# Kernel tuning notes

Measured on AMD Instinct MI355X. Metric: run time of the kernel, lower is better.

## Reference

```python
import jax, jax.numpy as jnp
import numpy as np

D_MODEL = 256
N_LAYERS = 2
EXPAND = 2
D_INNER = EXPAND * D_MODEL  # 512
D_STATE = 16
D_CONV = 4
DT_RANK = max(1, D_MODEL // 16)  # 16


def _selective_scan(x, dt, B, C, A, D):
    # x, dt: [b, l, d]   B, C: [b, l, n]   A: [d, n]   D: [d]
    dA = jnp.exp(jnp.einsum('bld,dn->bldn', dt, A))          # discretized state matrix
    dBx = jnp.einsum('bld,bln,bld->bldn', dt, B, x)           # dt * B * u

    def step(h, inp):
        dA_t, dBx_t, C_t = inp                                 # [b,d,n],[b,d,n],[b,n]
        h = dA_t * h + dBx_t
        y = jnp.einsum('bdn,bn->bd', h, C_t)
        return h, y

    h0 = jnp.zeros((x.shape[0], A.shape[0], A.shape[1]), x.dtype)
    _, ys = jax.lax.scan(step, h0, (jnp.moveaxis(dA, 1, 0),
                                    jnp.moveaxis(dBx, 1, 0),
                                    jnp.moveaxis(C, 1, 0)))
    return jnp.moveaxis(ys, 0, 1) + x * D                      # [b, l, d]


def _mamba_block(z, in_w, conv_w, conv_b, xp_w, dt_w, dt_b, A_log, Dp, out_w):
    b, l, _ = z.shape
    xz = z @ in_w.T                                            # [b, l, 2*d_inner]
    x, gate = jnp.split(xz, 2, axis=-1)
    # causal depthwise conv1d over time
    xt = jnp.transpose(x, (0, 2, 1))                            # [b, d_inner, l]
    xt = jax.lax.conv_general_dilated(
        xt, conv_w[:, None, :], window_strides=(1,),
        padding=[(D_CONV - 1, 0)], feature_group_count=D_INNER)
    x = jax.nn.silu(jnp.transpose(xt, (0, 2, 1)) + conv_b)      # [b, l, d_inner]
    x_dbl = x @ xp_w.T                                          # [b, l, dt_rank + 2*d_state]
    dt, Bm, Cm = jnp.split(x_dbl, [DT_RANK, DT_RANK + D_STATE], axis=-1)
    dt = jax.nn.softplus(dt @ dt_w.T + dt_b)                    # [b, l, d_inner]
    A = -jnp.exp(A_log)                                         # [d_inner, d_state]
    y = _selective_scan(x, dt, Bm, Cm, A, Dp)
    y = y * jax.nn.silu(gate)
    return y @ out_w.T                                          # [b, l, d_model]


def setup_inputs() -> dict:
    key = jax.random.key(0)
    ks = jax.random.split(key, 9)
    B, L = 2, 4096
    z = jax.random.normal(ks[0], (B, L, D_MODEL), jnp.float32)
    s = 0.02
    in_proj_w = jax.random.normal(ks[1], (N_LAYERS, 2 * D_INNER, D_MODEL), jnp.float32) * s
    conv_w = jax.random.normal(ks[2], (N_LAYERS, D_INNER, D_CONV), jnp.float32) * 0.2
    conv_b = jnp.zeros((N_LAYERS, D_INNER), jnp.float32)
    x_proj_w = jax.random.normal(ks[3], (N_LAYERS, DT_RANK + 2 * D_STATE, D_INNER), jnp.float32) * s
    dt_proj_w = jax.random.normal(ks[4], (N_LAYERS, D_INNER, DT_RANK), jnp.float32) * 0.1
    dt_proj_b = jax.random.uniform(ks[5], (N_LAYERS, D_INNER), jnp.float32, -4.0, -2.0)
    A_log = jnp.log(jnp.broadcast_to(jnp.arange(1, D_STATE + 1, dtype=jnp.float32),
                                     (N_LAYERS, D_INNER, D_STATE)))
    D_param = jnp.ones((N_LAYERS, D_INNER), jnp.float32)
    out_proj_w = jax.random.normal(ks[6], (N_LAYERS, D_MODEL, D_INNER), jnp.float32) * s
    return {"z": z, "in_proj_w": in_proj_w, "conv_w": conv_w, "conv_b": conv_b,
            "x_proj_w": x_proj_w, "dt_proj_w": dt_proj_w, "dt_proj_b": dt_proj_b,
            "A_log": A_log, "D_param": D_param, "out_proj_w": out_proj_w}


def reference(z, in_proj_w, conv_w, conv_b, x_proj_w, dt_proj_w, dt_proj_b,
              A_log, D_param, out_proj_w):
    for i in range(N_LAYERS):
        z = _mamba_block(z, in_proj_w[i], conv_w[i], conv_b[i], x_proj_w[i],
                         dt_proj_w[i], dt_proj_b[i], A_log[i], D_param[i], out_proj_w[i])
    return z
```

## Files before the change

### kernel.cpp

```cpp
#include <hip/hip_runtime.h>
#include <hip/hip_bf16.h>
#include <cstdint>
#include <cstddef>

#define DM   256
#define DI   512
#define DS   16
#define LSEQ 4096
#define BATCH 2
#define BLROWS (BATCH * LSEQ)
#define NCH  256
#define CLEN 16
#define NSC  16
#define XCP  520

typedef __bf16 bf16x8 __attribute__((ext_vector_type(8)));
typedef float  f32x4  __attribute__((ext_vector_type(4)));
typedef unsigned short u16;
typedef u16 u16x8 __attribute__((ext_vector_type(8)));

__device__ __forceinline__ u16 f2bfu(float f) {
    union { float f; unsigned u; } c; c.f = f;
    unsigned u = c.u;
    return (u16)((u + 0x7fffu + ((u >> 16) & 1u)) >> 16);
}
__device__ __forceinline__ float bfu2f(u16 u) {
    union { unsigned u; float f; } c; c.u = ((unsigned)u) << 16; return c.f;
}
__device__ __forceinline__ float siluf(float v) {
    return v * (1.0f / (1.0f + __expf(-v)));
}
__device__ __forceinline__ void gload_lds16(const void* g, void* l) {
    __builtin_amdgcn_global_load_lds(
        (const __attribute__((address_space(1))) unsigned int*)g,
        (__attribute__((address_space(3))) unsigned int*)l, 16, 0, 0);
}

#define POW_TREE(an, e1)                                                     \
    {   float e2 = (e1)*(e1), e4 = e2*e2, e8 = e4*e4;                        \
        an[0]=(e1); an[1]=e2; an[2]=e2*(e1); an[3]=e4; an[4]=e4*(e1);        \
        an[5]=e4*e2; an[6]=e4*an[2]; an[7]=e8; an[8]=e8*(e1); an[9]=e8*e2;   \
        an[10]=e8*an[2]; an[11]=e8*e4; an[12]=e8*an[4]; an[13]=e8*an[5];     \
        an[14]=e8*an[6]; an[15]=e8*e8; }

#define N_INW  (2*1024*256)
#define N_OUTW (2*256*512)
#define N_XPW  (2*64*512)
#define N_Z    (BLROWS*DM)
__global__ __launch_bounds__(256) void cast_all_k(
    const float* __restrict__ in_w, const float* __restrict__ out_w,
    const float* __restrict__ xp_w, const float* __restrict__ z,
    u16* __restrict__ inw_bf, u16* __restrict__ outw_bf,
    u16* __restrict__ xpw_bf, u16* __restrict__ z_bf) {
    int i = blockIdx.x * 256 + threadIdx.x;
    if (i < N_INW) {
        inw_bf[i] = f2bfu(in_w[i]);
    } else if (i < N_INW + N_OUTW) {
        int j = i - N_INW;
        outw_bf[j] = f2bfu(out_w[j]);
    } else if (i < N_INW + N_OUTW + N_XPW) {
        int j = i - (N_INW + N_OUTW);
        int k = j & 511, o = (j >> 9) & 63, l = j >> 15;
        xpw_bf[j] = f2bfu((o < 48) ? xp_w[(l * 48 + o) * 512 + k] : 0.0f);
    } else {
        int j = i - (N_INW + N_OUTW + N_XPW);
        z_bf[j] = f2bfu(z[j]);
    }
}

__global__ __launch_bounds__(256) void gemm_in_k(
    const __bf16* __restrict__ A, const __bf16* __restrict__ B,
    u16* __restrict__ Cb, int M, int N, int K) {
    __shared__ __bf16 As[128 * 32];
    __shared__ __bf16 Bs[128 * 32];
    int tid = threadIdx.x, wave = tid >> 6, lane = tid & 63;
    int bm = blockIdx.x * 128, bn = blockIdx.y * 128;
    int wm = (wave & 1) * 64, wn = (wave >> 1) * 64;
    int row = lane & 15, q = lane >> 4;
    int srow = lane >> 2, sseg = lane & 3;
    f32x4 acc[4][4] = {};
    for (int k0 = 0; k0 < K; k0 += 32) {
        #pragma unroll
        for (int i = 0; i < 2; ++i) {
            int r0 = wave * 32 + i * 16;
            gload_lds16(A + (size_t)(bm + r0 + srow) * K + k0 + sseg * 8, As + r0 * 32);
            gload_lds16(B + (size_t)(bn + r0 + srow) * K + k0 + sseg * 8, Bs + r0 * 32);
        }
        __syncthreads();
        bf16x8 af[4], bfr[4];
        #pragma unroll
        for (int mi = 0; mi < 4; ++mi)
            af[mi] = *(const bf16x8*)&As[(wm + mi*16 + row) * 32 + q * 8];
        #pragma unroll
        for (int ni = 0; ni < 4; ++ni)
            bfr[ni] = *(const bf16x8*)&Bs[(wn + ni*16 + row) * 32 + q * 8];
        #pragma unroll
        for (int mi = 0; mi < 4; ++mi)
            #pragma unroll
            for (int ni = 0; ni < 4; ++ni)
                acc[mi][ni] = __builtin_amdgcn_mfma_f32_16x16x32_bf16(
                    af[mi], bfr[ni], acc[mi][ni], 0, 0, 0);
        __syncthreads();
    }
    #pragma unroll
    for (int mi = 0; mi < 4; ++mi)
        #pragma unroll
        for (int r = 0; r < 4; ++r) {
            size_t gr = (size_t)(bm + wm + mi*16 + q*4 + r) * N;
            #pragma unroll
            for (int ni = 0; ni < 4; ++ni)
                Cb[gr + bn + wn + ni*16 + row] = f2bfu(acc[mi][ni][r]);
        }
}

__global__ __launch_bounds__(512, 6) void fused_a_k(
    const u16* __restrict__ xz, const float* __restrict__ cw,
    const float* __restrict__ cb, const __bf16* __restrict__ xpw,
    const float* __restrict__ dtw, const float* __restrict__ dtb,
    const float* __restrict__ Alog,
    u16* __restrict__ xcb, u16* __restrict__ dtob,
    float* __restrict__ BCg, u16* __restrict__ Pb, u16* __restrict__ Sb) {
    __shared__ u16 xc_s[CLEN * XCP];
    __shared__ float xd_h[2][CLEN * 68];
    int tid = threadIdx.x;
    int c = blockIdx.x, b = blockIdx.y;
    int flat = b * NCH + c;
    int bl0 = b * LSEQ + c * CLEN;
    int d = tid;

    {
        float w0 = cw[d*4], w1 = cw[d*4+1], w2 = cw[d*4+2], w3 = cw[d*4+3];
        float bias = cb[d];
        float xm3 = 0.f, xm2 = 0.f, xm1 = 0.f;
        int l0 = c * CLEN;
        if (l0 - 3 >= 0) xm3 = bfu2f(xz[(size_t)(bl0 - 3) * 1024 + d]);
        if (l0 - 2 >= 0) xm2 = bfu2f(xz[(size_t)(bl0 - 2) * 1024 + d]);
        if (l0 - 1 >= 0) xm1 = bfu2f(xz[(size_t)(bl0 - 1) * 1024 + d]);
        #pragma unroll 4
        for (int t = 0; t < CLEN; ++t) {
            float xcur = bfu2f(xz[(size_t)(bl0 + t) * 1024 + d]);
            float acc = fmaf(w0, xm3, fmaf(w1, xm2, fmaf(w2, xm1, fmaf(w3, xcur, bias))));
            float v = siluf(acc);
            u16 vb = f2bfu(v);
            xc_s[t * XCP + d] = vb;
            xcb[(size_t)(bl0 + t) * DI + d] = vb;
            xm3 = xm2; xm2 = xm1; xm1 = xcur;
        }
    }
    __syncthreads();

    {
        int wave = tid >> 6, lane = tid & 63;
        int row = lane & 15, q = lane >> 4;
        int nt = wave & 3, kh = wave >> 2;
        f32x4 acc = {0.f, 0.f, 0.f, 0.f};
        #pragma unroll
        for (int kb = 0; kb < 8; ++kb) {
            int kk = (kh*8 + kb) * 32;
            bf16x8 a = *(const bf16x8*)&xc_s[row * XCP + kk + q*8];
            bf16x8 bb = *(const bf16x8*)(xpw + (size_t)(nt*16 + row) * 512 + kk + q*8);
            acc = __builtin_amdgcn_mfma_f32_16x16x32_bf16(a, bb, acc, 0, 0, 0);
        }
        #pragma unroll
        for (int r = 0; r < 4; ++r)
            xd_h[kh][(q*4 + r) * 68 + nt*16 + row] = acc[r];
    }
    __syncthreads();
    for (int j = tid; j < CLEN * 68; j += 512) xd_h[0][j] += xd_h[1][j];
    __syncthreads();

    {
        int t = tid >> 5, cc = tid & 31;
        BCg[(size_t)flat * (CLEN*32) + tid] = xd_h[0][t*68 + 16 + cc];
    }

    {
        float dtwr[16];
        const f32x4* w4 = (const f32x4*)(dtw + (size_t)d * 16);
        #pragma unroll
        for (int g = 0; g < 4; ++g) { f32x4 v = w4[g];
            dtwr[g*4] = v[0]; dtwr[g*4+1] = v[1]; dtwr[g*4+2] = v[2]; dtwr[g*4+3] = v[3]; }
        float dtbv = dtb[d];
        float Ac0; bool fastp = true;
        {
            const f32x4* a4 = (const f32x4*)(Alog + (size_t)d * 16);
            f32x4 v0 = a4[0];
            Ac0 = -__expf(v0[0]);
            #pragma unroll
            for (int g = 0; g < 4; ++g) { f32x4 v = a4[g];
                #pragma unroll
                for (int j = 0; j < 4; ++j) { int n = g*4 + j; if (n) {
                    float acn = -__expf(v[j]);
                    fastp = fastp && (fabsf(acn - (float)(n+1)*Ac0) <= 1e-4f*fabsf(acn));
                } } }
        }
        float s[16];
        #pragma unroll
        for (int n = 0; n < 16; ++n) s[n] = 0.f;
        float Sdt = 0.f;
        if (fastp) {
            for (int t = 0; t < CLEN; ++t) {
                float acc = dtbv;
                #pragma unroll
                for (int r = 0; r < 16; ++r) acc = fmaf(xd_h[0][t*68 + r], dtwr[r], acc);
                float dtraw = (acc > 20.0f) ? acc : logf(1.0f + __expf(acc));
                u16 dtu = f2bfu(dtraw);
                dtob[(size_t)(bl0 + t) * DI + d] = dtu;
                float dtv = bfu2f(dtu);
                float xv = bfu2f(xc_s[t * XCP + d]);
                float dx = dtv * xv;
                Sdt += dtv;
                float e1 = __expf(dtv * Ac0);
                float an[16];
                POW_TREE(an, e1)
                #pragma unroll
                for (int n = 0; n < 16; ++n)
                    s[n] = fmaf(an[n], s[n], xd_h[0][t*68 + 16 + n] * dx);
            }
        } else {
            for (int t = 0; t < CLEN; ++t) {
                float acc = dtbv;
                #pragma unroll
                for (int r = 0; r < 16; ++r) acc = fmaf(xd_h[0][t*68 + r], dtwr[r], acc);
                float dtraw = (acc > 20.0f) ? acc : logf(1.0f + __expf(acc));
                u16 dtu = f2bfu(dtraw);
                dtob[(size_t)(bl0 + t) * DI + d] = dtu;
                float dtv = bfu2f(dtu);
                float xv = bfu2f(xc_s[t * XCP + d]);
                float dx = dtv * xv;
                Sdt += dtv;
                #pragma unroll
                for (int n = 0; n < 16; ++n) {
                    float an = __expf(dtv * -__expf(Alog[(size_t)d*16 + n]));
                    s[n] = fmaf(an, s[n], xd_h[0][t*68 + 16 + n] * dx);
                }
            }
        }
        float pw[16];
        if (fastp) {
            float E1 = __expf(Ac0 * Sdt);
            POW_TREE(pw, E1)
        } else {
            #pragma unroll
            for (int n = 0; n < 16; ++n)
                pw[n] = __expf(-__expf(Alog[(size_t)d*16 + n]) * Sdt);
        }
        size_t base = ((size_t)flat * DI + d) * 16;
        u16x8 pv0, pv1, sv0, sv1;
        #pragma unroll
        for (int n = 0; n < 8; ++n) {
            pv0[n] = f2bfu(pw[n]);  pv1[n] = f2bfu(pw[8+n]);
            sv0[n] = f2bfu(s[n]);   sv1[n] = f2bfu(s[8+n]);
        }
        *(u16x8*)(Pb + base)     = pv0;  *(u16x8*)(Pb + base + 8) = pv1;
        *(u16x8*)(Sb + base)     = sv0;  *(u16x8*)(Sb + base + 8) = sv1;
    }
}

__global__ __launch_bounds__(256) void scan1_k(
    const u16* __restrict__ Pb, const u16* __restrict__ Sb,
    float* __restrict__ Pagg, float* __restrict__ Sagg) {
    int gid = blockIdx.x * 256 + threadIdx.x;
    int scg = gid >> 13, elow = gid & 8191;
    int b = scg >> 4, sc = scg & 15;
    int cbase = b * NCH + sc * 16;
    float h = 0.f, p = 1.f;
    #pragma unroll
    for (int k = 0; k < 16; ++k) {
        size_t a = (size_t)(cbase + k) * 8192 + elow;
        float Pv = bfu2f(Pb[a]), Sv = bfu2f(Sb[a]);
        h = fmaf(Pv, h, Sv);
        p *= Pv;
    }
    Pagg[(size_t)scg * 8192 + elow] = p;
    Sagg[(size_t)scg * 8192 + elow] = h;
}

__global__ __launch_bounds__(256) void scan2_k(
    const u16* __restrict__ Pb, const u16* __restrict__ Sb,
    const float* __restrict__ Pagg, const float* __restrict__ Sagg,
    u16* __restrict__ Hg) {
    int gid = blockIdx.x * 256 + threadIdx.x;
    int scg = gid >> 13, elow = gid & 8191;
    int b = scg >> 4, sc = scg & 15;
    int cbase = b * NCH + sc * 16;
    float h = 0.f;
    for (int s2 = 0; s2 < sc; ++s2) {
        size_t ai = (size_t)(b*16 + s2) * 8192 + elow;
        h = fmaf(Pagg[ai], h, Sagg[ai]);
    }
    #pragma unroll
    for (int k = 0; k < 16; ++k) {
        size_t a = (size_t)(cbase + k) * 8192 + elow;
        Hg[a] = f2bfu(h);
        h = fmaf(bfu2f(Pb[a]), h, bfu2f(Sb[a]));
    }
}

__global__ __launch_bounds__(512, 6) void fused_c_k(
    const u16* __restrict__ xcb, const u16* __restrict__ dtob,
    const float* __restrict__ BCg, const u16* __restrict__ Hg,
    const float* __restrict__ Alog, const float* __restrict__ Dp,
    const u16* __restrict__ xz, const __bf16* __restrict__ outw,
    u16* __restrict__ Ob, float* __restrict__ Of) {
    __shared__ u16 y_s[CLEN * XCP];
    __shared__ float BCs[CLEN * 32];
    int tid = threadIdx.x;
    int c = blockIdx.x, b = blockIdx.y;
    int flat = b * NCH + c;
    int bl0 = b * LSEQ + c * CLEN;
    int d = tid;

    BCs[tid] = BCg[(size_t)flat * (CLEN*32) + tid];

    float Ac0; bool fastp = true;
    {
        const f32x4* a4 = (const f32x4*)(Alog + (size_t)d * 16);
        f32x4 v0 = a4[0];
        Ac0 = -__expf(v0[0]);
        #pragma unroll
        for (int g = 0; g < 4; ++g) { f32x4 v = a4[g];
            #pragma unroll
            for (int j = 0; j < 4; ++j) { int n = g*4 + j; if (n) {
                float acn = -__expf(v[j]);
                fastp = fastp && (fabsf(acn - (float)(n+1)*Ac0) <= 1e-4f*fabsf(acn));
            } } }
    }
    float h[16];
    {
        const u16* h8 = Hg + ((size_t)flat * DI + d) * 16;
        u16x8 hv0 = *(const u16x8*)h8;
        u16x8 hv1 = *(const u16x8*)(h8 + 8);
        #pragma unroll
        for (int n = 0; n < 8; ++n) { h[n] = bfu2f(hv0[n]); h[8+n] = bfu2f(hv1[n]); }
    }
    float Dv = Dp[d];
    __syncthreads();

    if (fastp) {
        for (int t = 0; t < CLEN; ++t) {
            float dtv = bfu2f(dtob[(size_t)(bl0 + t) * DI + d]);
            float xv  = bfu2f(xcb[(size_t)(bl0 + t) * DI + d]);
            float gv  = bfu2f(xz[(size_t)(bl0 + t) * 1024 + DI + d]);
            float dx = dtv * xv;
            float e1 = __expf(dtv * Ac0);
            float an[16];
            POW_TREE(an, e1)
            float y0 = 0.f, y1 = 0.f, y2 = 0.f, y3 = 0.f;
            #pragma unroll
            for (int n = 0; n < 4; ++n) {
                h[n]    = fmaf(an[n],    h[n],    BCs[t*32 + n]    * dx);
                h[4+n]  = fmaf(an[4+n],  h[4+n],  BCs[t*32 + 4+n]  * dx);
                h[8+n]  = fmaf(an[8+n],  h[8+n],  BCs[t*32 + 8+n]  * dx);
                h[12+n] = fmaf(an[12+n], h[12+n], BCs[t*32 + 12+n] * dx);
                y0 = fmaf(h[n],    BCs[t*32 + 16 + n],    y0);
                y1 = fmaf(h[4+n],  BCs[t*32 + 16 + 4+n],  y1);
                y2 = fmaf(h[8+n],  BCs[t*32 + 16 + 8+n],  y2);
                y3 = fmaf(h[12+n], BCs[t*32 + 16 + 12+n], y3);
            }
            float y = (y0 + y1) + (y2 + y3);
            float yv = fmaf(xv, Dv, y) * siluf(gv);
            y_s[t * XCP + d] = f2bfu(yv);
        }
    } else {
        for (int t = 0; t < CLEN; ++t) {
            float dtv = bfu2f(dtob[(size_t)(bl0 + t) * DI + d]);
            float xv  = bfu2f(xcb[(size_t)(bl0 + t) * DI + d]);
            float gv  = bfu2f(xz[(size_t)(bl0 + t) * 1024 + DI + d]);
            float dx = dtv * xv;
            float y = 0.f;
            #pragma unroll
            for (int n = 0; n < 16; ++n) {
                float an = __expf(dtv * -__expf(Alog[(size_t)d*16 + n]));
                h[n] = fmaf(an, h[n], BCs[t*32 + n] * dx);
                y = fmaf(h[n], BCs[t*32 + 16 + n], y);
            }
            float yv = fmaf(xv, Dv, y) * siluf(gv);
            y_s[t * XCP + d] = f2bfu(yv);
        }
    }
    __syncthreads();

    {
        int wave = tid >> 6, lane = tid & 63;
        int row = lane & 15, q = lane >> 4;
        f32x4 acc[2] = {};
        #pragma unroll
        for (int kb = 0; kb < 16; ++kb) {
            bf16x8 a = *(const bf16x8*)&y_s[row * XCP + kb*32 + q*8];
            #pragma unroll
            for (int ni = 0; ni < 2; ++ni) {
                bf16x8 bb = *(const bf16x8*)(outw +
                    (size_t)(wave*32 + ni*16 + row) * 512 + kb*32 + q*8);
                acc[ni] = __builtin_amdgcn_mfma_f32_16x16x32_bf16(a, bb, acc[ni], 0, 0, 0);
            }
        }
        #pragma unroll
        for (int r = 0; r < 4; ++r) {
            size_t gr = (size_t)(bl0 + q*4 + r) * DM;
            #pragma unroll
            for (int ni = 0; ni < 2; ++ni) {
                int gc = wave*32 + ni*16 + row;
                if (Ob) Ob[gr + gc] = f2bfu(acc[ni][r]);
                else    Of[gr + gc] = acc[ni][r];
            }
        }
    }
}

extern "C" void kernel_launch(void* const* d_in, const int* in_sizes, int n_in,
                              void* d_out, int out_size, void* d_ws, size_t ws_size,
                              hipStream_t stream) {
    (void)in_sizes; (void)n_in; (void)out_size; (void)ws_size;
    const float* z_in   = (const float*)d_in[0];
    const float* in_w   = (const float*)d_in[1];
    const float* conv_w = (const float*)d_in[2];
    const float* conv_b = (const float*)d_in[3];
    const float* xp_w   = (const float*)d_in[4];
    const float* dt_w   = (const float*)d_in[5];
    const float* dt_b   = (const float*)d_in[6];
    const float* A_log  = (const float*)d_in[7];
    const float* D_par  = (const float*)d_in[8];
    const float* out_w  = (const float*)d_in[9];
    float* outp = (float*)d_out;

    char* p = (char*)d_ws;
    auto alloc = [&](size_t bytes) { char* r = p; p += (bytes + 255) & ~(size_t)255; return r; };
    u16* z_bf    = (u16*)alloc((size_t)BLROWS*DM*2);
    u16* z2_bf   = (u16*)alloc((size_t)BLROWS*DM*2);
    u16* xz_bf   = (u16*)alloc((size_t)BLROWS*1024*2);
    u16* xc_bf   = (u16*)alloc((size_t)BLROWS*DI*2);
    u16* dt_bf   = (u16*)alloc((size_t)BLROWS*DI*2);
    u16* inw_bf  = (u16*)alloc((size_t)2*1024*256*2);
    u16* outw_bf = (u16*)alloc((size_t)2*256*512*2);
    u16* xpw_bf  = (u16*)alloc((size_t)2*64*512*2);
    float* BCg   = (float*)alloc((size_t)BATCH*NCH*CLEN*32*4);
    u16* Pbuf    = (u16*)alloc((size_t)BATCH*NCH*DI*DS*2);
    u16* Sbuf    = (u16*)alloc((size_t)BATCH*NCH*DI*DS*2);
    u16* Hbuf    = (u16*)alloc((size_t)BATCH*NCH*DI*DS*2);
    float* PaggG = (float*)alloc((size_t)BATCH*NSC*8192*4);
    float* SaggG = (float*)alloc((size_t)BATCH*NSC*8192*4);

    cast_all_k<<<(N_INW + N_OUTW + N_XPW + N_Z)/256, 256, 0, stream>>>(
        in_w, out_w, xp_w, z_in, inw_bf, outw_bf, xpw_bf, z_bf);

    const u16* zcur = z_bf;
    for (int l = 0; l < 2; ++l) {
        gemm_in_k<<<dim3(BLROWS/128, 1024/128), 256, 0, stream>>>(
            (const __bf16*)zcur, (const __bf16*)(inw_bf + (size_t)l*1024*256),
            xz_bf, BLROWS, 1024, 256);
        fused_a_k<<<dim3(NCH, BATCH), 512, 0, stream>>>(
            xz_bf, conv_w + (size_t)l*DI*4, conv_b + (size_t)l*DI,
            (const __bf16*)(xpw_bf + (size_t)l*64*512),
            dt_w + (size_t)l*DI*16, dt_b + (size_t)l*DI,
            A_log + (size_t)l*DI*DS,
            xc_bf, dt_bf, BCg, Pbuf, Sbuf);
        scan1_k<<<BATCH*NSC*8192/256, 256, 0, stream>>>(Pbuf, Sbuf, PaggG, SaggG);
        scan2_k<<<BATCH*NSC*8192/256, 256, 0, stream>>>(Pbuf, Sbuf, PaggG, SaggG, Hbuf);
        fused_c_k<<<dim3(NCH, BATCH), 512, 0, stream>>>(
            xc_bf, dt_bf, BCg, Hbuf,
            A_log + (size_t)l*DI*DS, D_par + (size_t)l*DI,
            xz_bf, (const __bf16*)(outw_bf + (size_t)l*256*512),
            (l == 0) ? z2_bf : nullptr, (l == 1) ? outp : nullptr);
        zcur = z2_bf;
    }
}
```

Measured before the change: 234.0 us.

## Fuse input projection GEMM into chunk kernel and merge the two scan passes

The separate in-projection GEMM is removed. Each fused_a_k block now computes its own 16-row chunk plus an 8-row causal halo of the x projection directly into LDS, and writes only the gate half to global memory, so the full xz tensor is no longer written and re-read. The two inter-chunk scan kernels are merged into one block-level kernel that keeps per-chunk P/S values in registers and combines super-chunk aggregates through shared memory. In exchange, each block recomputes halo rows (the GEMM does 32 rows per 16 used), reads in_proj weights straight from global without LDS tiling, and occupancy of fused_a_k drops to 4 blocks per CU.

```diff
diff --git a/kernel.cpp b/kernel.cpp
--- a/kernel.cpp
+++ b/kernel.cpp
@@ -29,11 +29,6 @@
 }
 __device__ __forceinline__ float siluf(float v) {
     return v * (1.0f / (1.0f + __expf(-v)));
-}
-__device__ __forceinline__ void gload_lds16(const void* g, void* l) {
-    __builtin_amdgcn_global_load_lds(
-        (const __attribute__((address_space(1))) unsigned int*)g,
-        (__attribute__((address_space(3))) unsigned int*)l, 16, 0, 0);
 }
 
 #define POW_TREE(an, e1)                                                     \
@@ -68,85 +63,92 @@
     }
 }
 
-__global__ __launch_bounds__(256) void gemm_in_k(
-    const __bf16* __restrict__ A, const __bf16* __restrict__ B,
-    u16* __restrict__ Cb, int M, int N, int K) {
-    __shared__ __bf16 As[128 * 32];
-    __shared__ __bf16 Bs[128 * 32];
-    int tid = threadIdx.x, wave = tid >> 6, lane = tid & 63;
-    int bm = blockIdx.x * 128, bn = blockIdx.y * 128;
-    int wm = (wave & 1) * 64, wn = (wave >> 1) * 64;
-    int row = lane & 15, q = lane >> 4;
-    int srow = lane >> 2, sseg = lane & 3;
-    f32x4 acc[4][4] = {};
-    for (int k0 = 0; k0 < K; k0 += 32) {
-        #pragma unroll
-        for (int i = 0; i < 2; ++i) {
-            int r0 = wave * 32 + i * 16;
-            gload_lds16(A + (size_t)(bm + r0 + srow) * K + k0 + sseg * 8, As + r0 * 32);
-            gload_lds16(B + (size_t)(bn + r0 + srow) * K + k0 + sseg * 8, Bs + r0 * 32);
-        }
-        __syncthreads();
-        bf16x8 af[4], bfr[4];
-        #pragma unroll
-        for (int mi = 0; mi < 4; ++mi)
-            af[mi] = *(const bf16x8*)&As[(wm + mi*16 + row) * 32 + q * 8];
-        #pragma unroll
-        for (int ni = 0; ni < 4; ++ni)
-            bfr[ni] = *(const bf16x8*)&Bs[(wn + ni*16 + row) * 32 + q * 8];
-        #pragma unroll
-        for (int mi = 0; mi < 4; ++mi)
-            #pragma unroll
-            for (int ni = 0; ni < 4; ++ni)
-                acc[mi][ni] = __builtin_amdgcn_mfma_f32_16x16x32_bf16(
-                    af[mi], bfr[ni], acc[mi][ni], 0, 0, 0);
-        __syncthreads();
-    }
-    #pragma unroll
-    for (int mi = 0; mi < 4; ++mi)
-        #pragma unroll
-        for (int r = 0; r < 4; ++r) {
-            size_t gr = (size_t)(bm + wm + mi*16 + q*4 + r) * N;
-            #pragma unroll
-            for (int ni = 0; ni < 4; ++ni)
-                Cb[gr + bn + wn + ni*16 + row] = f2bfu(acc[mi][ni][r]);
-        }
-}
-
-__global__ __launch_bounds__(512, 6) void fused_a_k(
-    const u16* __restrict__ xz, const float* __restrict__ cw,
-    const float* __restrict__ cb, const __bf16* __restrict__ xpw,
+__global__ __launch_bounds__(512, 4) void fused_a_k(
+    const __bf16* __restrict__ Az, const __bf16* __restrict__ inw,
+    const float* __restrict__ cw, const float* __restrict__ cb,
+    const __bf16* __restrict__ xpw,
     const float* __restrict__ dtw, const float* __restrict__ dtb,
     const float* __restrict__ Alog,
-    u16* __restrict__ xcb, u16* __restrict__ dtob,
+    u16* __restrict__ gate, u16* __restrict__ xcb, u16* __restrict__ dtob,
     float* __restrict__ BCg, u16* __restrict__ Pb, u16* __restrict__ Sb) {
-    __shared__ u16 xc_s[CLEN * XCP];
-    __shared__ float xd_h[2][CLEN * 68];
+    __shared__ u16 smem[32 * XCP];
+    float* xd = (float*)&smem[16 * XCP];
     int tid = threadIdx.x;
     int c = blockIdx.x, b = blockIdx.y;
     int flat = b * NCH + c;
     int bl0 = b * LSEQ + c * CLEN;
+    int l0 = c * CLEN;
     int d = tid;
 
+    {
+        int wave = tid >> 6, lane = tid & 63;
+        int r15 = lane & 15, q = lane >> 4;
+        int ng = wave;
+        int ar0 = bl0 - 8 + r15; if (ar0 < 0) ar0 = 0;
+        int ar1 = bl0 + 8 + r15; if (ar1 > BLROWS - 1) ar1 = BLROWS - 1;
+        const __bf16* Ap0 = Az + (size_t)ar0 * 256 + q * 8;
+        const __bf16* Ap1 = Az + (size_t)ar1 * 256 + q * 8;
+        #pragma unroll
+        for (int pass = 0; pass < 2; ++pass) {
+            int ncol = ng * 128 + pass * 64;
+            f32x4 acc[2][4] = {};
+            #pragma unroll
+            for (int k = 0; k < 8; ++k) {
+                bf16x8 a0 = *(const bf16x8*)(Ap0 + k * 32);
+                bf16x8 a1 = *(const bf16x8*)(Ap1 + k * 32);
+                #pragma unroll
+                for (int ni = 0; ni < 4; ++ni) {
+                    bf16x8 bf = *(const bf16x8*)(inw +
+                        (size_t)(ncol + ni*16 + r15) * 256 + k*32 + q*8);
+                    acc[0][ni] = __builtin_amdgcn_mfma_f32_16x16x32_bf16(a0, bf, acc[0][ni], 0, 0, 0);
+                    acc[1][ni] = __builtin_amdgcn_mfma_f32_16x16x32_bf16(a1, bf, acc[1][ni], 0, 0, 0);
+                }
+            }
+            if (ng < 4) {
+                #pragma unroll
+                for (int mt = 0; mt < 2; ++mt)
+                    #pragma unroll
+                    for (int ni = 0; ni < 4; ++ni)
+                        #pragma unroll
+                        for (int r = 0; r < 4; ++r)
+                            smem[(mt*16 + q*4 + r) * XCP + ncol + ni*16 + r15] =
+                                f2bfu(acc[mt][ni][r]);
+            } else {
+                #pragma unroll
+                for (int mt = 0; mt < 2; ++mt)
+                    #pragma unroll
+                    for (int ni = 0; ni < 4; ++ni)
+                        #pragma unroll
+                        for (int r = 0; r < 4; ++r) {
+                            int ro = mt*16 + q*4 + r;
+                            if (ro >= 8 && ro < 24)
+                                gate[(size_t)(bl0 + ro - 8) * 512 +
+                                     (ncol - 512) + ni*16 + r15] = f2bfu(acc[mt][ni][r]);
+                        }
+            }
+        }
+    }
+    __syncthreads();
+
+    u16 vb[CLEN];
     {
         float w0 = cw[d*4], w1 = cw[d*4+1], w2 = cw[d*4+2], w3 = cw[d*4+3];
         float bias = cb[d];
-        float xm3 = 0.f, xm2 = 0.f, xm1 = 0.f;
-        int l0 = c * CLEN;
-        if (l0 - 3 >= 0) xm3 = bfu2f(xz[(size_t)(bl0 - 3) * 1024 + d]);
-        if (l0 - 2 >= 0) xm2 = bfu2f(xz[(size_t)(bl0 - 2) * 1024 + d]);
-        if (l0 - 1 >= 0) xm1 = bfu2f(xz[(size_t)(bl0 - 1) * 1024 + d]);
-        #pragma unroll 4
+        float xm3 = (l0 >= 3) ? bfu2f(smem[5 * XCP + d]) : 0.f;
+        float xm2 = (l0 >= 2) ? bfu2f(smem[6 * XCP + d]) : 0.f;
+        float xm1 = (l0 >= 1) ? bfu2f(smem[7 * XCP + d]) : 0.f;
+        #pragma unroll
         for (int t = 0; t < CLEN; ++t) {
-            float xcur = bfu2f(xz[(size_t)(bl0 + t) * 1024 + d]);
+            float xcur = bfu2f(smem[(8 + t) * XCP + d]);
             float acc = fmaf(w0, xm3, fmaf(w1, xm2, fmaf(w2, xm1, fmaf(w3, xcur, bias))));
-            float v = siluf(acc);
-            u16 vb = f2bfu(v);
-            xc_s[t * XCP + d] = vb;
-            xcb[(size_t)(bl0 + t) * DI + d] = vb;
+            vb[t] = f2bfu(siluf(acc));
+            xcb[(size_t)(bl0 + t) * DI + d] = vb[t];
             xm3 = xm2; xm2 = xm1; xm1 = xcur;
         }
     }
+    __syncthreads();
+    #pragma unroll
+    for (int t = 0; t < CLEN; ++t) smem[t * XCP + d] = vb[t];
     __syncthreads();
 
     {
@@ -157,21 +159,21 @@
         #pragma unroll
         for (int kb = 0; kb < 8; ++kb) {
             int kk = (kh*8 + kb) * 32;
-            bf16x8 a = *(const bf16x8*)&xc_s[row * XCP + kk + q*8];
+            bf16x8 a = *(const bf16x8*)&smem[row * XCP + kk + q*8];
             bf16x8 bb = *(const bf16x8*)(xpw + (size_t)(nt*16 + row) * 512 + kk + q*8);
             acc = __builtin_amdgcn_mfma_f32_16x16x32_bf16(a, bb, acc, 0, 0, 0);
         }
         #pragma unroll
         for (int r = 0; r < 4; ++r)
-            xd_h[kh][(q*4 + r) * 68 + nt*16 + row] = acc[r];
-    }
-    __syncthreads();
-    for (int j = tid; j < CLEN * 68; j += 512) xd_h[0][j] += xd_h[1][j];
+            xd[kh * (CLEN*68) + (q*4 + r) * 68 + nt*16 + row] = acc[r];
+    }
+    __syncthreads();
+    for (int j = tid; j < CLEN * 68; j += 512) xd[j] += xd[CLEN*68 + j];
     __syncthreads();
 
     {
         int t = tid >> 5, cc = tid & 31;
-        BCg[(size_t)flat * (CLEN*32) + tid] = xd_h[0][t*68 + 16 + cc];
+        BCg[(size_t)flat * (CLEN*32) + tid] = xd[t*68 + 16 + cc];
     }
 
     {
@@ -199,15 +201,16 @@
         for (int n = 0; n < 16; ++n) s[n] = 0.f;
         float Sdt = 0.f;
         if (fastp) {
+            #pragma unroll
             for (int t = 0; t < CLEN; ++t) {
                 float acc = dtbv;
                 #pragma unroll
-                for (int r = 0; r < 16; ++r) acc = fmaf(xd_h[0][t*68 + r], dtwr[r], acc);
+                for (int r = 0; r < 16; ++r) acc = fmaf(xd[t*68 + r], dtwr[r], acc);
                 float dtraw = (acc > 20.0f) ? acc : logf(1.0f + __expf(acc));
                 u16 dtu = f2bfu(dtraw);
                 dtob[(size_t)(bl0 + t) * DI + d] = dtu;
                 float dtv = bfu2f(dtu);
-                float xv = bfu2f(xc_s[t * XCP + d]);
+                float xv = bfu2f(vb[t]);
                 float dx = dtv * xv;
                 Sdt += dtv;
                 float e1 = __expf(dtv * Ac0);
@@ -215,24 +218,25 @@
                 POW_TREE(an, e1)
                 #pragma unroll
                 for (int n = 0; n < 16; ++n)
-                    s[n] = fmaf(an[n], s[n], xd_h[0][t*68 + 16 + n] * dx);
+                    s[n] = fmaf(an[n], s[n], xd[t*68 + 16 + n] * dx);
             }
         } else {
+            #pragma unroll
             for (int t = 0; t < CLEN; ++t) {
                 float acc = dtbv;
                 #pragma unroll
-                for (int r = 0; r < 16; ++r) acc = fmaf(xd_h[0][t*68 + r], dtwr[r], acc);
+                for (int r = 0; r < 16; ++r) acc = fmaf(xd[t*68 + r], dtwr[r], acc);
                 float dtraw = (acc > 20.0f) ? acc : logf(1.0f + __expf(acc));
                 u16 dtu = f2bfu(dtraw);
                 dtob[(size_t)(bl0 + t) * DI + d] = dtu;
                 float dtv = bfu2f(dtu);
-                float xv = bfu2f(xc_s[t * XCP + d]);
+                float xv = bfu2f(vb[t]);
                 float dx = dtv * xv;
                 Sdt += dtv;
                 #pragma unroll
                 for (int n = 0; n < 16; ++n) {
                     float an = __expf(dtv * -__expf(Alog[(size_t)d*16 + n]));
-                    s[n] = fmaf(an, s[n], xd_h[0][t*68 + 16 + n] * dx);
+                    s[n] = fmaf(an, s[n], xd[t*68 + 16 + n] * dx);
                 }
             }
         }
@@ -257,43 +261,34 @@
     }
 }
 
-__global__ __launch_bounds__(256) void scan1_k(
+__global__ __launch_bounds__(1024) void scan12_k(
     const u16* __restrict__ Pb, const u16* __restrict__ Sb,
-    float* __restrict__ Pagg, float* __restrict__ Sagg) {
-    int gid = blockIdx.x * 256 + threadIdx.x;
-    int scg = gid >> 13, elow = gid & 8191;
-    int b = scg >> 4, sc = scg & 15;
+    u16* __restrict__ Hg) {
+    __shared__ float pag[NSC][64], sag[NSC][64];
+    int tid = threadIdx.x;
+    int eo = tid & 63, sc = tid >> 6;
+    int elow = blockIdx.x * 64 + eo;
+    int b = blockIdx.y;
     int cbase = b * NCH + sc * 16;
+    float Pr[16], Sr[16];
     float h = 0.f, p = 1.f;
     #pragma unroll
     for (int k = 0; k < 16; ++k) {
         size_t a = (size_t)(cbase + k) * 8192 + elow;
-        float Pv = bfu2f(Pb[a]), Sv = bfu2f(Sb[a]);
-        h = fmaf(Pv, h, Sv);
-        p *= Pv;
-    }
-    Pagg[(size_t)scg * 8192 + elow] = p;
-    Sagg[(size_t)scg * 8192 + elow] = h;
-}
-
-__global__ __launch_bounds__(256) void scan2_k(
-    const u16* __restrict__ Pb, const u16* __restrict__ Sb,
-    const float* __restrict__ Pagg, const float* __restrict__ Sagg,
-    u16* __restrict__ Hg) {
-    int gid = blockIdx.x * 256 + threadIdx.x;
-    int scg = gid >> 13, elow = gid & 8191;
-    int b = scg >> 4, sc = scg & 15;
-    int cbase = b * NCH + sc * 16;
-    float h = 0.f;
-    for (int s2 = 0; s2 < sc; ++s2) {
-        size_t ai = (size_t)(b*16 + s2) * 8192 + elow;
-        h = fmaf(Pagg[ai], h, Sagg[ai]);
-    }
+        Pr[k] = bfu2f(Pb[a]); Sr[k] = bfu2f(Sb[a]);
+        h = fmaf(Pr[k], h, Sr[k]);
+        p *= Pr[k];
+    }
+    pag[sc][eo] = p; sag[sc][eo] = h;
+    __syncthreads();
+    float hs = 0.f;
+    for (int s2 = 0; s2 < sc; ++s2)
+        hs = fmaf(pag[s2][eo], hs, sag[s2][eo]);
     #pragma unroll
     for (int k = 0; k < 16; ++k) {
         size_t a = (size_t)(cbase + k) * 8192 + elow;
-        Hg[a] = f2bfu(h);
-        h = fmaf(bfu2f(Pb[a]), h, bfu2f(Sb[a]));
+        Hg[a] = f2bfu(hs);
+        hs = fmaf(Pr[k], hs, Sr[k]);
     }
 }
 
@@ -301,7 +296,7 @@
     const u16* __restrict__ xcb, const u16* __restrict__ dtob,
     const float* __restrict__ BCg, const u16* __restrict__ Hg,
     const float* __restrict__ Alog, const float* __restrict__ Dp,
-    const u16* __restrict__ xz, const __bf16* __restrict__ outw,
+    const u16* __restrict__ gate, const __bf16* __restrict__ outw,
     u16* __restrict__ Ob, float* __restrict__ Of) {
     __shared__ u16 y_s[CLEN * XCP];
     __shared__ float BCs[CLEN * 32];
@@ -341,7 +336,7 @@
         for (int t = 0; t < CLEN; ++t) {
             float dtv = bfu2f(dtob[(size_t)(bl0 + t) * DI + d]);
             float xv  = bfu2f(xcb[(size_t)(bl0 + t) * DI + d]);
-            float gv  = bfu2f(xz[(size_t)(bl0 + t) * 1024 + DI + d]);
+            float gv  = bfu2f(gate[(size_t)(bl0 + t) * 512 + d]);
             float dx = dtv * xv;
             float e1 = __expf(dtv * Ac0);
             float an[16];
@@ -366,7 +361,7 @@
         for (int t = 0; t < CLEN; ++t) {
             float dtv = bfu2f(dtob[(size_t)(bl0 + t) * DI + d]);
             float xv  = bfu2f(xcb[(size_t)(bl0 + t) * DI + d]);
-            float gv  = bfu2f(xz[(size_t)(bl0 + t) * 1024 + DI + d]);
+            float gv  = bfu2f(gate[(size_t)(bl0 + t) * 512 + d]);
             float dx = dtv * xv;
             float y = 0.f;
             #pragma unroll
@@ -428,7 +423,7 @@
     auto alloc = [&](size_t bytes) { char* r = p; p += (bytes + 255) & ~(size_t)255; return r; };
     u16* z_bf    = (u16*)alloc((size_t)BLROWS*DM*2);
     u16* z2_bf   = (u16*)alloc((size_t)BLROWS*DM*2);
-    u16* xz_bf   = (u16*)alloc((size_t)BLROWS*1024*2);
+    u16* gate_bf = (u16*)alloc((size_t)BLROWS*DI*2);
     u16* xc_bf   = (u16*)alloc((size_t)BLROWS*DI*2);
     u16* dt_bf   = (u16*)alloc((size_t)BLROWS*DI*2);
     u16* inw_bf  = (u16*)alloc((size_t)2*1024*256*2);
@@ -438,29 +433,24 @@
     u16* Pbuf    = (u16*)alloc((size_t)BATCH*NCH*DI*DS*2);
     u16* Sbuf    = (u16*)alloc((size_t)BATCH*NCH*DI*DS*2);
     u16* Hbuf    = (u16*)alloc((size_t)BATCH*NCH*DI*DS*2);
-    float* PaggG = (float*)alloc((size_t)BATCH*NSC*8192*4);
-    float* SaggG = (float*)alloc((size_t)BATCH*NSC*8192*4);
 
     cast_all_k<<<(N_INW + N_OUTW + N_XPW + N_Z)/256, 256, 0, stream>>>(
         in_w, out_w, xp_w, z_in, inw_bf, outw_bf, xpw_bf, z_bf);
 
     const u16* zcur = z_bf;
     for (int l = 0; l < 2; ++l) {
-        gemm_in_k<<<dim3(BLROWS/128, 1024/128), 256, 0, stream>>>(
+        fused_a_k<<<dim3(NCH, BATCH), 512, 0, stream>>>(
             (const __bf16*)zcur, (const __bf16*)(inw_bf + (size_t)l*1024*256),
-            xz_bf, BLROWS, 1024, 256);
-        fused_a_k<<<dim3(NCH, BATCH), 512, 0, stream>>>(
-            xz_bf, conv_w + (size_t)l*DI*4, conv_b + (size_t)l*DI,
+            conv_w + (size_t)l*DI*4, conv_b + (size_t)l*DI,
             (const __bf16*)(xpw_bf + (size_t)l*64*512),
             dt_w + (size_t)l*DI*16, dt_b + (size_t)l*DI,
             A_log + (size_t)l*DI*DS,
-            xc_bf, dt_bf, BCg, Pbuf, Sbuf);
-        scan1_k<<<BATCH*NSC*8192/256, 256, 0, stream>>>(Pbuf, Sbuf, PaggG, SaggG);
-        scan2_k<<<BATCH*NSC*8192/256, 256, 0, stream>>>(Pbuf, Sbuf, PaggG, SaggG, Hbuf);
+            gate_bf, xc_bf, dt_bf, BCg, Pbuf, Sbuf);
+        scan12_k<<<dim3(8192/64, BATCH), 1024, 0, stream>>>(Pbuf, Sbuf, Hbuf);
         fused_c_k<<<dim3(NCH, BATCH), 512, 0, stream>>>(
             xc_bf, dt_bf, BCg, Hbuf,
             A_log + (size_t)l*DI*DS, D_par + (size_t)l*DI,
-            xz_bf, (const __bf16*)(outw_bf + (size_t)l*256*512),
+            gate_bf, (const __bf16*)(outw_bf + (size_t)l*256*512),
             (l == 0) ? z2_bf : nullptr, (l == 1) ? outp : nullptr);
         zcur = z2_bf;
     }
```

Measured after the change: 309.3 us. 1.32x slower.

## Merge scan passes into one kernel and pack dt with conv output

Applied to the files above, without the earlier changes.

Replaces the two-pass chunk-aggregate scan (scan1/scan2 with global Pagg/Sagg buffers) with a single kernel that holds each sub-chunk's P/S values in registers and combines sub-chunk aggregates through shared memory. This removes one launch, the global aggregate buffers and the re-read of P/S. It also packs the bf16 dt and conv outputs into one u32 array, so the consumer kernel issues one load per element instead of two. The per-timestep loops are fully unrolled and use vectorized float4 reads from shared memory in both fused kernels. The cost is 1024-thread blocks with 32 extra registers per thread.

```diff
diff --git a/kernel.cpp b/kernel.cpp
--- a/kernel.cpp
+++ b/kernel.cpp
@@ -17,6 +17,7 @@
 typedef __bf16 bf16x8 __attribute__((ext_vector_type(8)));
 typedef float  f32x4  __attribute__((ext_vector_type(4)));
 typedef unsigned short u16;
+typedef unsigned int u32;
 typedef u16 u16x8 __attribute__((ext_vector_type(8)));
 
 __device__ __forceinline__ u16 f2bfu(float f) {
@@ -118,16 +119,17 @@
     const float* __restrict__ cb, const __bf16* __restrict__ xpw,
     const float* __restrict__ dtw, const float* __restrict__ dtb,
     const float* __restrict__ Alog,
-    u16* __restrict__ xcb, u16* __restrict__ dtob,
-    float* __restrict__ BCg, u16* __restrict__ Pb, u16* __restrict__ Sb) {
+    u32* __restrict__ dxc, float* __restrict__ BCg,
+    u16* __restrict__ Pb, u16* __restrict__ Sb) {
     __shared__ u16 xc_s[CLEN * XCP];
-    __shared__ float xd_h[2][CLEN * 68];
+    __shared__ __attribute__((aligned(16))) float xd_h[2][CLEN * 68];
     int tid = threadIdx.x;
     int c = blockIdx.x, b = blockIdx.y;
     int flat = b * NCH + c;
     int bl0 = b * LSEQ + c * CLEN;
     int d = tid;
 
+    u16 vb[CLEN];
     {
         float w0 = cw[d*4], w1 = cw[d*4+1], w2 = cw[d*4+2], w3 = cw[d*4+3];
         float bias = cb[d];
@@ -136,14 +138,12 @@
         if (l0 - 3 >= 0) xm3 = bfu2f(xz[(size_t)(bl0 - 3) * 1024 + d]);
         if (l0 - 2 >= 0) xm2 = bfu2f(xz[(size_t)(bl0 - 2) * 1024 + d]);
         if (l0 - 1 >= 0) xm1 = bfu2f(xz[(size_t)(bl0 - 1) * 1024 + d]);
-        #pragma unroll 4
+        #pragma unroll
         for (int t = 0; t < CLEN; ++t) {
             float xcur = bfu2f(xz[(size_t)(bl0 + t) * 1024 + d]);
             float acc = fmaf(w0, xm3, fmaf(w1, xm2, fmaf(w2, xm1, fmaf(w3, xcur, bias))));
-            float v = siluf(acc);
-            u16 vb = f2bfu(v);
-            xc_s[t * XCP + d] = vb;
-            xcb[(size_t)(bl0 + t) * DI + d] = vb;
+            vb[t] = f2bfu(siluf(acc));
+            xc_s[t * XCP + d] = vb[t];
             xm3 = xm2; xm2 = xm1; xm1 = xcur;
         }
     }
@@ -175,11 +175,11 @@
     }
 
     {
-        float dtwr[16];
-        const f32x4* w4 = (const f32x4*)(dtw + (size_t)d * 16);
-        #pragma unroll
-        for (int g = 0; g < 4; ++g) { f32x4 v = w4[g];
-            dtwr[g*4] = v[0]; dtwr[g*4+1] = v[1]; dtwr[g*4+2] = v[2]; dtwr[g*4+3] = v[3]; }
+        f32x4 w0, w1, w2, w3;
+        {
+            const f32x4* w4 = (const f32x4*)(dtw + (size_t)d * 16);
+            w0 = w4[0]; w1 = w4[1]; w2 = w4[2]; w3 = w4[3];
+        }
         float dtbv = dtb[d];
         float Ac0; bool fastp = true;
         {
@@ -198,42 +198,39 @@
         #pragma unroll
         for (int n = 0; n < 16; ++n) s[n] = 0.f;
         float Sdt = 0.f;
-        if (fastp) {
-            for (int t = 0; t < CLEN; ++t) {
-                float acc = dtbv;
-                #pragma unroll
-                for (int r = 0; r < 16; ++r) acc = fmaf(xd_h[0][t*68 + r], dtwr[r], acc);
-                float dtraw = (acc > 20.0f) ? acc : logf(1.0f + __expf(acc));
-                u16 dtu = f2bfu(dtraw);
-                dtob[(size_t)(bl0 + t) * DI + d] = dtu;
-                float dtv = bfu2f(dtu);
-                float xv = bfu2f(xc_s[t * XCP + d]);
-                float dx = dtv * xv;
-                Sdt += dtv;
+        #pragma unroll
+        for (int t = 0; t < CLEN; ++t) {
+            const f32x4* xr = (const f32x4*)&xd_h[0][t * 68];
+            f32x4 x0 = xr[0], x1 = xr[1], x2 = xr[2], x3 = xr[3];
+            float acc = dtbv;
+            #pragma unroll
+            for (int j = 0; j < 4; ++j) {
+                acc = fmaf(x0[j], w0[j], acc); acc = fmaf(x1[j], w1[j], acc);
+                acc = fmaf(x2[j], w2[j], acc); acc = fmaf(x3[j], w3[j], acc);
+            }
+            float dtraw = (acc > 20.0f) ? acc : logf(1.0f + __expf(acc));
+            u16 dtu = f2bfu(dtraw);
+            float dtv = bfu2f(dtu);
+            dxc[(size_t)(bl0 + t) * DI + d] = ((u32)dtu << 16) | (u32)vb[t];
+            float xv = bfu2f(vb[t]);
+            float dx = dtv * xv;
+            Sdt += dtv;
+            f32x4 b0 = xr[4], b1 = xr[5], b2 = xr[6], b3 = xr[7];
+            float an[16];
+            if (fastp) {
                 float e1 = __expf(dtv * Ac0);
-                float an[16];
                 POW_TREE(an, e1)
+            } else {
                 #pragma unroll
                 for (int n = 0; n < 16; ++n)
-                    s[n] = fmaf(an[n], s[n], xd_h[0][t*68 + 16 + n] * dx);
+                    an[n] = __expf(dtv * -__expf(Alog[(size_t)d*16 + n]));
             }
-        } else {
-            for (int t = 0; t < CLEN; ++t) {
-                float acc = dtbv;
-                #pragma unroll
-                for (int r = 0; r < 16; ++r) acc = fmaf(xd_h[0][t*68 + r], dtwr[r], acc);
-                float dtraw = (acc > 20.0f) ? acc : logf(1.0f + __expf(acc));
-                u16 dtu = f2bfu(dtraw);
-                dtob[(size_t)(bl0 + t) * DI + d] = dtu;
-                float dtv = bfu2f(dtu);
-                float xv = bfu2f(xc_s[t * XCP + d]);
-                float dx = dtv * xv;
-                Sdt += dtv;
-                #pragma unroll
-                for (int n = 0; n < 16; ++n) {
-                    float an = __expf(dtv * -__expf(Alog[(size_t)d*16 + n]));
-                    s[n] = fmaf(an, s[n], xd_h[0][t*68 + 16 + n] * dx);
-                }
+            #pragma unroll
+            for (int j = 0; j < 4; ++j) {
+                s[j]    = fmaf(an[j],    s[j],    b0[j] * dx);
+                s[4+j]  = fmaf(an[4+j],  s[4+j],  b1[j] * dx);
+                s[8+j]  = fmaf(an[8+j],  s[8+j],  b2[j] * dx);
+                s[12+j] = fmaf(an[12+j], s[12+j], b3[j] * dx);
             }
         }
         float pw[16];
@@ -257,54 +254,45 @@
     }
 }
 
-__global__ __launch_bounds__(256) void scan1_k(
+__global__ __launch_bounds__(1024) void scan12_k(
     const u16* __restrict__ Pb, const u16* __restrict__ Sb,
-    float* __restrict__ Pagg, float* __restrict__ Sagg) {
-    int gid = blockIdx.x * 256 + threadIdx.x;
-    int scg = gid >> 13, elow = gid & 8191;
-    int b = scg >> 4, sc = scg & 15;
+    u16* __restrict__ Hg) {
+    __shared__ float pag[NSC][64], sag[NSC][64];
+    int tid = threadIdx.x;
+    int eo = tid & 63, sc = tid >> 6;
+    int elow = blockIdx.x * 64 + eo;
+    int b = blockIdx.y;
     int cbase = b * NCH + sc * 16;
+    float Pr[16], Sr[16];
     float h = 0.f, p = 1.f;
     #pragma unroll
     for (int k = 0; k < 16; ++k) {
         size_t a = (size_t)(cbase + k) * 8192 + elow;
-        float Pv = bfu2f(Pb[a]), Sv = bfu2f(Sb[a]);
-        h = fmaf(Pv, h, Sv);
-        p *= Pv;
-    }
-    Pagg[(size_t)scg * 8192 + elow] = p;
-    Sagg[(size_t)scg * 8192 + elow] = h;
-}
-
-__global__ __launch_bounds__(256) void scan2_k(
-    const u16* __restrict__ Pb, const u16* __restrict__ Sb,
-    const float* __restrict__ Pagg, const float* __restrict__ Sagg,
-    u16* __restrict__ Hg) {
-    int gid = blockIdx.x * 256 + threadIdx.x;
-    int scg = gid >> 13, elow = gid & 8191;
-    int b = scg >> 4, sc = scg & 15;
-    int cbase = b * NCH + sc * 16;
-    float h = 0.f;
-    for (int s2 = 0; s2 < sc; ++s2) {
-        size_t ai = (size_t)(b*16 + s2) * 8192 + elow;
-        h = fmaf(Pagg[ai], h, Sagg[ai]);
-    }
+        Pr[k] = bfu2f(Pb[a]); Sr[k] = bfu2f(Sb[a]);
+        h = fmaf(Pr[k], h, Sr[k]);
+        p *= Pr[k];
+    }
+    pag[sc][eo] = p; sag[sc][eo] = h;
+    __syncthreads();
+    float hs = 0.f;
+    for (int s2 = 0; s2 < sc; ++s2)
+        hs = fmaf(pag[s2][eo], hs, sag[s2][eo]);
     #pragma unroll
     for (int k = 0; k < 16; ++k) {
         size_t a = (size_t)(cbase + k) * 8192 + elow;
-        Hg[a] = f2bfu(h);
-        h = fmaf(bfu2f(Pb[a]), h, bfu2f(Sb[a]));
+        Hg[a] = f2bfu(hs);
+        hs = fmaf(Pr[k], hs, Sr[k]);
     }
 }
 
 __global__ __launch_bounds__(512, 6) void fused_c_k(
-    const u16* __restrict__ xcb, const u16* __restrict__ dtob,
-    const float* __restrict__ BCg, const u16* __restrict__ Hg,
+    const u32* __restrict__ dxc, const float* __restrict__ BCg,
+    const u16* __restrict__ Hg,
     const float* __restrict__ Alog, const float* __restrict__ Dp,
     const u16* __restrict__ xz, const __bf16* __restrict__ outw,
     u16* __restrict__ Ob, float* __restrict__ Of) {
     __shared__ u16 y_s[CLEN * XCP];
-    __shared__ float BCs[CLEN * 32];
+    __shared__ __attribute__((aligned(16))) float BCs[CLEN * 32];
     int tid = threadIdx.x;
     int c = blockIdx.x, b = blockIdx.y;
     int flat = b * NCH + c;
@@ -337,47 +325,40 @@
     float Dv = Dp[d];
     __syncthreads();
 
-    if (fastp) {
-        for (int t = 0; t < CLEN; ++t) {
-            float dtv = bfu2f(dtob[(size_t)(bl0 + t) * DI + d]);
-            float xv  = bfu2f(xcb[(size_t)(bl0 + t) * DI + d]);
-            float gv  = bfu2f(xz[(size_t)(bl0 + t) * 1024 + DI + d]);
-            float dx = dtv * xv;
+    #pragma unroll
+    for (int t = 0; t < CLEN; ++t) {
+        u32 dxv = dxc[(size_t)(bl0 + t) * DI + d];
+        float dtv = bfu2f((u16)(dxv >> 16));
+        float xv  = bfu2f((u16)(dxv & 0xffffu));
+        float gv  = bfu2f(xz[(size_t)(bl0 + t) * 1024 + DI + d]);
+        float dx = dtv * xv;
+        const f32x4* br = (const f32x4*)&BCs[t * 32];
+        f32x4 b0 = br[0], b1 = br[1], b2 = br[2], b3 = br[3];
+        f32x4 c0 = br[4], c1 = br[5], c2 = br[6], c3 = br[7];
+        float an[16];
+        if (fastp) {
             float e1 = __expf(dtv * Ac0);
-            float an[16];
             POW_TREE(an, e1)
-            float y0 = 0.f, y1 = 0.f, y2 = 0.f, y3 = 0.f;
-            #pragma unroll
-            for (int n = 0; n < 4; ++n) {
-                h[n]    = fmaf(an[n],    h[n],    BCs[t*32 + n]    * dx);
-                h[4+n]  = fmaf(an[4+n],  h[4+n],  BCs[t*32 + 4+n]  * dx);
-                h[8+n]  = fmaf(an[8+n],  h[8+n],  BCs[t*32 + 8+n]  * dx);
-                h[12+n] = fmaf(an[12+n], h[12+n], BCs[t*32 + 12+n] * dx);
-                y0 = fmaf(h[n],    BCs[t*32 + 16 + n],    y0);
-                y1 = fmaf(h[4+n],  BCs[t*32 + 16 + 4+n],  y1);
-                y2 = fmaf(h[8+n],  BCs[t*32 + 16 + 8+n],  y2);
-                y3 = fmaf(h[12+n], BCs[t*32 + 16 + 12+n], y3);
-            }
-            float y = (y0 + y1) + (y2 + y3);
-            float yv = fmaf(xv, Dv, y) * siluf(gv);
-            y_s[t * XCP + d] = f2bfu(yv);
-        }
-    } else {
-        for (int t = 0; t < CLEN; ++t) {
-            float dtv = bfu2f(dtob[(size_t)(bl0 + t) * DI + d]);
-            float xv  = bfu2f(xcb[(size_t)(bl0 + t) * DI + d]);
-            float gv  = bfu2f(xz[(size_t)(bl0 + t) * 1024 + DI + d]);
-            float dx = dtv * xv;
-            float y = 0.f;
-            #pragma unroll
-            for (int n = 0; n < 16; ++n) {
-                float an = __expf(dtv * -__expf(Alog[(size_t)d*16 + n]));
-                h[n] = fmaf(an, h[n], BCs[t*32 + n] * dx);
-                y = fmaf(h[n], BCs[t*32 + 16 + n], y);
-            }
-            float yv = fmaf(xv, Dv, y) * siluf(gv);
-            y_s[t * XCP + d] = f2bfu(yv);
-        }
+        } else {
+            #pragma unroll
+            for (int n = 0; n < 16; ++n)
+                an[n] = __expf(dtv * -__expf(Alog[(size_t)d*16 + n]));
+        }
+        float y0 = 0.f, y1 = 0.f, y2 = 0.f, y3 = 0.f;
+        #pragma unroll
+        for (int j = 0; j < 4; ++j) {
+            h[j]    = fmaf(an[j],    h[j],    b0[j] * dx);
+            h[4+j]  = fmaf(an[4+j],  h[4+j],  b1[j] * dx);
+            h[8+j]  = fmaf(an[8+j],  h[8+j],  b2[j] * dx);
+            h[12+j] = fmaf(an[12+j], h[12+j], b3[j] * dx);
+            y0 = fmaf(h[j],    c0[j], y0);
+            y1 = fmaf(h[4+j],  c1[j], y1);
+            y2 = fmaf(h[8+j],  c2[j], y2);
+            y3 = fmaf(h[12+j], c3[j], y3);
+        }
+        float y = (y0 + y1) + (y2 + y3);
+        float yv = fmaf(xv, Dv, y) * siluf(gv);
+        y_s[t * XCP + d] = f2bfu(yv);
     }
     __syncthreads();
 
@@ -429,8 +410,7 @@
     u16* z_bf    = (u16*)alloc((size_t)BLROWS*DM*2);
     u16* z2_bf   = (u16*)alloc((size_t)BLROWS*DM*2);
     u16* xz_bf   = (u16*)alloc((size_t)BLROWS*1024*2);
-    u16* xc_bf   = (u16*)alloc((size_t)BLROWS*DI*2);
-    u16* dt_bf   = (u16*)alloc((size_t)BLROWS*DI*2);
+    u32* dxc_bf  = (u32*)alloc((size_t)BLROWS*DI*4);
     u16* inw_bf  = (u16*)alloc((size_t)2*1024*256*2);
     u16* outw_bf = (u16*)alloc((size_t)2*256*512*2);
     u16* xpw_bf  = (u16*)alloc((size_t)2*64*512*2);
@@ -438,8 +418,6 @@
     u16* Pbuf    = (u16*)alloc((size_t)BATCH*NCH*DI*DS*2);
     u16* Sbuf    = (u16*)alloc((size_t)BATCH*NCH*DI*DS*2);
     u16* Hbuf    = (u16*)alloc((size_t)BATCH*NCH*DI*DS*2);
-    float* PaggG = (float*)alloc((size_t)BATCH*NSC*8192*4);
-    float* SaggG = (float*)alloc((size_t)BATCH*NSC*8192*4);
 
     cast_all_k<<<(N_INW + N_OUTW + N_XPW + N_Z)/256, 256, 0, stream>>>(
         in_w, out_w, xp_w, z_in, inw_bf, outw_bf, xpw_bf, z_bf);
@@ -454,11 +432,10 @@
             (const __bf16*)(xpw_bf + (size_t)l*64*512),
             dt_w + (size_t)l*DI*16, dt_b + (size_t)l*DI,
             A_log + (size_t)l*DI*DS,
-            xc_bf, dt_bf, BCg, Pbuf, Sbuf);
-        scan1_k<<<BATCH*NSC*8192/256, 256, 0, stream>>>(Pbuf, Sbuf, PaggG, SaggG);
-        scan2_k<<<BATCH*NSC*8192/256, 256, 0, stream>>>(Pbuf, Sbuf, PaggG, SaggG, Hbuf);
+            dxc_bf, BCg, Pbuf, Sbuf);
+        scan12_k<<<dim3(8192/64, BATCH), 1024, 0, stream>>>(Pbuf, Sbuf, Hbuf);
         fused_c_k<<<dim3(NCH, BATCH), 512, 0, stream>>>(
-            xc_bf, dt_bf, BCg, Hbuf,
+            dxc_bf, BCg, Hbuf,
             A_log + (size_t)l*DI*DS, D_par + (size_t)l*DI,
             xz_bf, (const __bf16*)(outw_bf + (size_t)l*256*512),
             (l == 0) ? z2_bf : nullptr, (l == 1) ? outp : nullptr);
```

Result: slower. 808.7 us (+245.6%).
